# Performance work log

Measured on AMD Instinct MI355X. Metric: run time of the kernel, lower is better.

Reference implementation:

```python
import jax, jax.numpy as jnp
import numpy as np

B, S, HID, NH, HS = 4, 1024, 4096, 32, 128
ROT = 64  # rotary dim = head_size // 2 (ChatGLM partial rotary)
BLOCK_SIZE = 128


def setup_inputs() -> dict:
    key = jax.random.key(0)
    k0, k1, k2 = jax.random.split(key, 3)
    T = B * S
    hidden_states = jax.random.normal(k0, (T, HID), dtype=jnp.float32)
    w_qkv = jax.random.normal(k1, (HID, 3 * HID), dtype=jnp.float32) * 0.02
    b_qkv = jnp.zeros((3 * HID,), dtype=jnp.float32)
    w_dense = jax.random.normal(k2, (HID, HID), dtype=jnp.float32) * 0.02
    # real rotary tables: per-token position within its sequence
    inv_freq = 1.0 / (10000.0 ** (jnp.arange(0, ROT, 2, dtype=jnp.float32) / ROT))  # [ROT/2]
    pos = jnp.tile(jnp.arange(S, dtype=jnp.float32), B)  # [T]
    ang = pos[:, None] * inv_freq[None, :]  # [T, ROT/2]
    cos, sin = jnp.cos(ang), jnp.sin(ang)
    block_num = T // BLOCK_SIZE
    kv_cache_k = jnp.zeros((block_num, BLOCK_SIZE, NH, HS), dtype=jnp.float32)
    kv_cache_v = jnp.zeros((block_num, BLOCK_SIZE, NH, HS), dtype=jnp.float32)
    slots = jnp.arange(T, dtype=jnp.int32)
    return {"hidden_states": hidden_states, "cos": cos, "sin": sin,
            "w_qkv": w_qkv, "b_qkv": b_qkv, "w_dense": w_dense,
            "kv_cache_k": kv_cache_k, "kv_cache_v": kv_cache_v,
            "slots": slots, "batch": B, "seq_len": S}


def _rotary(x, cos, sin):
    # x: [T, NH, HS]; rotate-half over first ROT dims, pass-through the rest
    half = ROT // 2
    x1, x2, xp = x[..., :half], x[..., half:ROT], x[..., ROT:]
    c, s = cos[:, None, :], sin[:, None, :]
    return jnp.concatenate([x1 * c - x2 * s, x2 * c + x1 * s, xp], axis=-1)


def reference(hidden_states, cos, sin, w_qkv, b_qkv, w_dense,
              kv_cache_k, kv_cache_v, slots, batch, seq_len):
    T = hidden_states.shape[0]
    qkv = hidden_states @ w_qkv + b_qkv  # [T, 3*HID]
    q, k, v = jnp.split(qkv, 3, axis=1)
    q = q.reshape(T, NH, HS)
    k = k.reshape(T, NH, HS)
    v = v.reshape(T, NH, HS)
    q = _rotary(q, cos, sin)
    k = _rotary(k, cos, sin)
    # paged KV-cache scatter write (vectorized reshape_and_cache)
    bs = kv_cache_k.shape[1]
    bi, bo = slots // bs, slots % bs
    kv_k = kv_cache_k.at[bi, bo].set(k)
    kv_v = kv_cache_v.at[bi, bo].set(v)
    # prefill causal attention per sequence
    scale = HS ** -0.5
    q4 = q.reshape(batch, seq_len, NH, HS)
    k4 = k.reshape(batch, seq_len, NH, HS)
    v4 = v.reshape(batch, seq_len, NH, HS)
    scores = jnp.einsum("bqhd,bkhd->bhqk", q4, k4) * scale
    causal = jnp.tril(jnp.ones((seq_len, seq_len), dtype=bool))
    scores = jnp.where(causal[None, None], scores, jnp.finfo(scores.dtype).min)
    probs = jax.nn.softmax(scores, axis=-1)
    attn = jnp.einsum("bhqk,bkhd->bqhd", probs, v4).reshape(T, NH * HS)
    out = attn @ w_dense
    return out, kv_k, kv_v
```

## Files before the change

kernel.cpp:

```cpp
#include <hip/hip_runtime.h>

#define S_LEN 1024
#define NHEAD 32
#define HSZ   128
#define HIDN  4096
#define NQKV  12288
#define T_TOK 4096
#define ATT_SCALE 0.12751743f

typedef __bf16 bf16x8 __attribute__((ext_vector_type(8)));
typedef float  floatx4 __attribute__((ext_vector_type(4)));

union B8U { uint4 u; bf16x8 v; };

__device__ __forceinline__ unsigned short f2bf(float x) {
  unsigned int u = __float_as_uint(x);
  unsigned int r = (u + 0x7FFFu + ((u >> 16) & 1u)) >> 16;
  return (unsigned short)r;
}

__device__ __forceinline__ void gload_lds16(const void* g, void* l) {
  __builtin_amdgcn_global_load_lds(
      (__attribute__((address_space(1))) void*)(unsigned long long)g,
      (__attribute__((address_space(3))) void*)l, 16, 0, 0);
}

__device__ __forceinline__ bf16x8 lds_frag(const unsigned short* p) {
  return *reinterpret_cast<const bf16x8*>(p);
}

__global__ __launch_bounds__(256) void cast_bf16_kernel(
    const float* __restrict__ in, unsigned short* __restrict__ out, int n) {
  int idx = (blockIdx.x * 256 + threadIdx.x) * 4;
  if (idx >= n) return;
  float4 f = *reinterpret_cast<const float4*>(in + idx);
  ushort4 o;
  o.x = f2bf(f.x); o.y = f2bf(f.y); o.z = f2bf(f.z); o.w = f2bf(f.w);
  *reinterpret_cast<ushort4*>(out + idx) = o;
}

__global__ __launch_bounds__(256) void tcast_kernel(
    const float* __restrict__ w, unsigned short* __restrict__ wt, int K, int N) {
  __shared__ float tile[32][33];
  int n0 = blockIdx.x * 32, k0 = blockIdx.y * 32;
  int tx = threadIdx.x, ty = threadIdx.y;
#pragma unroll
  for (int i = 0; i < 32; i += 8)
    tile[ty + i][tx] = w[(size_t)(k0 + ty + i) * N + n0 + tx];
  __syncthreads();
#pragma unroll
  for (int i = 0; i < 32; i += 8)
    wt[(size_t)(n0 + ty + i) * K + k0 + tx] = f2bf(tile[tx][ty + i]);
}

__global__ __launch_bounds__(256) void gemm_bt(
    const unsigned short* __restrict__ A, const unsigned short* __restrict__ Bt,
    const float* __restrict__ bias, float* __restrict__ C, int M, int N, int K) {
  __shared__ __align__(16) unsigned short ldsA[128 * 32];
  __shared__ __align__(16) unsigned short ldsB[128 * 32];
  const int tid = threadIdx.x;
  const int lane = tid & 63, w = tid >> 6;
  const int m = lane & 15, quad = lane >> 4;
  const int wm = w >> 1, wn = w & 1;
  const int tM = blockIdx.y * 128, tN = blockIdx.x * 128;

  floatx4 acc[4][4] = {};
  const unsigned short* pA = A + (size_t)tM * K;
  const unsigned short* pB = Bt + (size_t)tN * K;
  const int r0 = tid >> 2, c0 = (tid & 3) * 8;

  for (int k0 = 0; k0 < K; k0 += 32) {
    gload_lds16(pA + (size_t)r0 * K + k0 + c0,        &ldsA[tid * 8]);
    gload_lds16(pA + (size_t)(r0 + 64) * K + k0 + c0, &ldsA[(tid + 256) * 8]);
    gload_lds16(pB + (size_t)r0 * K + k0 + c0,        &ldsB[tid * 8]);
    gload_lds16(pB + (size_t)(r0 + 64) * K + k0 + c0, &ldsB[(tid + 256) * 8]);
    __syncthreads();
    bf16x8 af[4], bfr[4];
#pragma unroll
    for (int i = 0; i < 4; ++i)
      af[i] = lds_frag(&ldsA[(wm * 64 + i * 16 + m) * 32 + quad * 8]);
#pragma unroll
    for (int j = 0; j < 4; ++j)
      bfr[j] = lds_frag(&ldsB[(wn * 64 + j * 16 + m) * 32 + quad * 8]);
#pragma unroll
    for (int i = 0; i < 4; ++i)
#pragma unroll
      for (int j = 0; j < 4; ++j)
        acc[i][j] = __builtin_amdgcn_mfma_f32_16x16x32_bf16(af[i], bfr[j], acc[i][j], 0, 0, 0);
    __syncthreads();
  }
#pragma unroll
  for (int i = 0; i < 4; ++i) {
    int row = tM + wm * 64 + i * 16 + quad * 4;
#pragma unroll
    for (int j = 0; j < 4; ++j) {
      int col = tN + wn * 64 + j * 16 + m;
      float bb = bias ? bias[col] : 0.0f;
      float* cp = C + (size_t)row * N + col;
#pragma unroll
      for (int r = 0; r < 4; ++r)
        cp[(size_t)r * N] = acc[i][j][r] + bb;
    }
  }
}

__global__ __launch_bounds__(256) void rope_kernel(
    const float* __restrict__ qkv, const float* __restrict__ cosb,
    const float* __restrict__ sinb, const int* __restrict__ slots,
    unsigned short* __restrict__ Qb, unsigned short* __restrict__ Kb,
    float* __restrict__ KvK, float* __restrict__ KvV) {
  const int t = blockIdx.x, tid = threadIdx.x;
  const size_t base = (size_t)t * NQKV;
  const int slot = slots[t];
  const size_t obase = (size_t)t * 4096;
  const size_t cbase = (size_t)slot * 4096;
  for (int idx = tid; idx < NHEAD * 32; idx += 256) {
    int hh = idx >> 5, r = idx & 31;
    float c = cosb[t * 32 + r], sn = sinb[t * 32 + r];
    int d0 = hh * 128 + r;
    float q1 = qkv[base + d0], q2 = qkv[base + d0 + 32];
    float k1 = qkv[base + 4096 + d0], k2 = qkv[base + 4096 + d0 + 32];
    float qr1 = q1 * c - q2 * sn, qr2 = q2 * c + q1 * sn;
    float kr1 = k1 * c - k2 * sn, kr2 = k2 * c + k1 * sn;
    Qb[obase + d0]      = f2bf(qr1 * ATT_SCALE);
    Qb[obase + d0 + 32] = f2bf(qr2 * ATT_SCALE);
    Kb[obase + d0]      = f2bf(kr1);
    Kb[obase + d0 + 32] = f2bf(kr2);
    KvK[cbase + d0] = kr1; KvK[cbase + d0 + 32] = kr2;
  }
  for (int idx = tid; idx < NHEAD * 64; idx += 256) {
    int hh = idx >> 6, p = idx & 63;
    int d = hh * 128 + 64 + p;
    float q = qkv[base + d], k = qkv[base + 4096 + d];
    Qb[obase + d] = f2bf(q * ATT_SCALE);
    Kb[obase + d] = f2bf(k);
    KvK[cbase + d] = k;
  }
  for (int idx = tid; idx < NHEAD * 128; idx += 256)
    KvV[cbase + idx] = qkv[base + 8192 + idx];
}

__global__ __launch_bounds__(256) void vtrans_kernel(
    const float* __restrict__ qkv, unsigned short* __restrict__ vt) {
  __shared__ float tile[32][33];
  int s0 = blockIdx.x * 32, d0 = blockIdx.y * 32, bh = blockIdx.z;
  int b = bh >> 5, h = bh & 31;
  int tx = threadIdx.x, ty = threadIdx.y;
#pragma unroll
  for (int i = 0; i < 32; i += 8)
    tile[ty + i][tx] =
        qkv[(size_t)(b * S_LEN + s0 + ty + i) * NQKV + 8192 + h * 128 + d0 + tx];
  __syncthreads();
#pragma unroll
  for (int i = 0; i < 32; i += 8)
    vt[(size_t)(bh * 128 + d0 + ty + i) * S_LEN + s0 + tx] = f2bf(tile[tx][ty + i]);
}

__global__ __launch_bounds__(256) void attn_kernel(
    const unsigned short* __restrict__ Q, const unsigned short* __restrict__ Kb,
    const unsigned short* __restrict__ Vt, unsigned short* __restrict__ Ob) {
  __shared__ __align__(16) unsigned short Ks[32][136];
  __shared__ __align__(16) unsigned short Vs[128][40];
  __shared__ __align__(16) unsigned short Pb[4][16][40];

  const int tid = threadIdx.x;
  const int w = tid >> 6, lane = tid & 63;
  const int m = lane & 15, quad = lane >> 4;
  const int qb = blockIdx.x, bh = blockIdx.y;
  const int b = bh >> 5, h = bh & 31;

  const int rowA = qb * 64 + w * 16 + m;
  const size_t qoff = ((size_t)(b * S_LEN + rowA)) * 4096 + h * 128;

  bf16x8 qf[4];
#pragma unroll
  for (int kc = 0; kc < 4; ++kc) {
    B8U t; t.u = *reinterpret_cast<const uint4*>(Q + qoff + kc * 32 + quad * 8);
    qf[kc] = t.v;
  }

  floatx4 O[8] = {};
  float m_run[4], l_run[4], alpha[4];
#pragma unroll
  for (int r = 0; r < 4; ++r) { m_run[r] = -3e38f; l_run[r] = 0.0f; }

  const int kend = qb * 64 + 63;
  for (int k0 = 0; k0 <= kend; k0 += 32) {
#pragma unroll
    for (int it = 0; it < 2; ++it) {
      int c = tid + it * 256;
      int key = c >> 4, d0 = (c & 15) * 8;
      uint4 val = *reinterpret_cast<const uint4*>(
          Kb + ((size_t)(b * S_LEN + k0 + key)) * 4096 + h * 128 + d0);
      *reinterpret_cast<uint4*>(&Ks[key][d0]) = val;
    }
#pragma unroll
    for (int it = 0; it < 2; ++it) {
      int c = tid + it * 256;
      int d = c >> 2, kk = (c & 3) * 8;
      uint4 val = *reinterpret_cast<const uint4*>(
          Vt + ((size_t)bh * 128 + d) * S_LEN + k0 + kk);
      *reinterpret_cast<uint4*>(&Vs[d][kk]) = val;
    }
    __syncthreads();

    floatx4 s[2];
#pragma unroll
    for (int t16 = 0; t16 < 2; ++t16) {
      floatx4 a = {};
#pragma unroll
      for (int kc = 0; kc < 4; ++kc) {
        bf16x8 kf = lds_frag(&Ks[t16 * 16 + m][kc * 32 + quad * 8]);
        a = __builtin_amdgcn_mfma_f32_16x16x32_bf16(qf[kc], kf, a, 0, 0, 0);
      }
      s[t16] = a;
    }

#pragma unroll
    for (int r = 0; r < 4; ++r) {
      int rowD = qb * 64 + w * 16 + quad * 4 + r;
      float s0 = s[0][r]; if (k0 + m > rowD)      s0 = -3e38f;
      float s1 = s[1][r]; if (k0 + 16 + m > rowD) s1 = -3e38f;
      float mx = fmaxf(s0, s1);
#pragma unroll
      for (int off = 8; off > 0; off >>= 1) mx = fmaxf(mx, __shfl_xor(mx, off));
      float mn = fmaxf(m_run[r], mx);
      float al = exp2f(m_run[r] - mn);
      float p0 = exp2f(s0 - mn), p1 = exp2f(s1 - mn);
      float rs = p0 + p1;
#pragma unroll
      for (int off = 8; off > 0; off >>= 1) rs += __shfl_xor(rs, off);
      l_run[r] = l_run[r] * al + rs;
      m_run[r] = mn; alpha[r] = al;
      Pb[w][quad * 4 + r][m]      = f2bf(p0);
      Pb[w][quad * 4 + r][16 + m] = f2bf(p1);
    }

#pragma unroll
    for (int nd = 0; nd < 8; ++nd)
#pragma unroll
      for (int r = 0; r < 4; ++r) O[nd][r] *= alpha[r];

    bf16x8 pf = lds_frag(&Pb[w][m][quad * 8]);
#pragma unroll
    for (int nd = 0; nd < 8; ++nd) {
      bf16x8 vf = lds_frag(&Vs[nd * 16 + m][quad * 8]);
      O[nd] = __builtin_amdgcn_mfma_f32_16x16x32_bf16(pf, vf, O[nd], 0, 0, 0);
    }
    __syncthreads();
  }

#pragma unroll
  for (int r = 0; r < 4; ++r) {
    int rowD = qb * 64 + w * 16 + quad * 4 + r;
    float inv = 1.0f / l_run[r];
    size_t obase = ((size_t)(b * S_LEN + rowD)) * 4096 + h * 128;
#pragma unroll
    for (int nd = 0; nd < 8; ++nd)
      Ob[obase + nd * 16 + m] = f2bf(O[nd][r] * inv);
  }
}

extern "C" void kernel_launch(void* const* d_in, const int* in_sizes, int n_in,
                              void* d_out, int out_size, void* d_ws, size_t ws_size,
                              hipStream_t stream) {
  const float* hidden  = (const float*)d_in[0];
  const float* cosb    = (const float*)d_in[1];
  const float* sinb    = (const float*)d_in[2];
  const float* w_qkv   = (const float*)d_in[3];
  const float* b_qkv   = (const float*)d_in[4];
  const float* w_dense = (const float*)d_in[5];
  const int*   slots   = (const int*)d_in[8];

  float* out = (float*)d_out;
  float* kvk = out + 16777216;
  float* kvv = out + 33554432;

  char* ws = (char*)d_ws;
  unsigned short* bfA = (unsigned short*)ws;
  unsigned short* Wt  = (unsigned short*)(ws + 33554432);
  float*          qkv = (float*)(ws + 134217728);
  unsigned short* Qb  = (unsigned short*)(ws + 335544320);
  unsigned short* Kb  = (unsigned short*)(ws + 369098752);
  unsigned short* Vt  = (unsigned short*)(ws + 402653184);

  cast_bf16_kernel<<<16384, 256, 0, stream>>>(hidden, bfA, T_TOK * HIDN);
  tcast_kernel<<<dim3(NQKV / 32, HIDN / 32), dim3(32, 8), 0, stream>>>(w_qkv, Wt, HIDN, NQKV);
  gemm_bt<<<dim3(NQKV / 128, T_TOK / 128), 256, 0, stream>>>(bfA, Wt, b_qkv, qkv, T_TOK, NQKV, HIDN);
  rope_kernel<<<T_TOK, 256, 0, stream>>>(qkv, cosb, sinb, slots, Qb, Kb, kvk, kvv);
  vtrans_kernel<<<dim3(S_LEN / 32, HSZ / 32, 128), dim3(32, 8), 0, stream>>>(qkv, Vt);
  attn_kernel<<<dim3(S_LEN / 64, 128), 256, 0, stream>>>(Qb, Kb, Vt, bfA);
  tcast_kernel<<<dim3(HIDN / 32, HIDN / 32), dim3(32, 8), 0, stream>>>(w_dense, Wt, HIDN, HIDN);
  gemm_bt<<<dim3(HIDN / 128, T_TOK / 128), 256, 0, stream>>>(bfA, Wt, nullptr, out, T_TOK, HIDN, HIDN);
}
```

Baseline: 1.561 ms.

## Replace 128x128 GEMM with pipelined 256x256 double-buffered swizzled LDS kernel

Replaces the simple 128x128-tile bf16 GEMM, which synchronised on every k-step, with a 256x256-tile, 512-thread kernel. It double-buffers LDS, issues staged async global-to-LDS loads interleaved with MFMA quarters, uses XOR-swizzled LDS layout to avoid bank conflicts, remaps workgroups for XCD/L2 locality, and raises wave priority during MFMA bursts. The goal is to hide memory latency and improve data reuse in both projection GEMMs. The cost is more LDS (128KB per block) and register pressure, plus fragile hand-placed waitcnt and barrier logic.

Measured after the change: 1.317 ms. 15.6% less time.

```diff
diff --git a/kernel.cpp b/kernel.cpp
--- a/kernel.cpp
+++ b/kernel.cpp
@@ -53,55 +53,162 @@
     wt[(size_t)(n0 + ty + i) * K + k0 + tx] = f2bf(tile[tx][ty + i]);
 }
 
-__global__ __launch_bounds__(256) void gemm_bt(
+__global__ __launch_bounds__(512, 2) void gemm256(
     const unsigned short* __restrict__ A, const unsigned short* __restrict__ Bt,
-    const float* __restrict__ bias, float* __restrict__ C, int M, int N, int K) {
-  __shared__ __align__(16) unsigned short ldsA[128 * 32];
-  __shared__ __align__(16) unsigned short ldsB[128 * 32];
+    const float* __restrict__ bias, float* __restrict__ C,
+    int N, int K, int NBX) {
+  __shared__ __align__(16) unsigned short ldsA[2][16384];
+  __shared__ __align__(16) unsigned short ldsB[2][16384];
+
   const int tid = threadIdx.x;
   const int lane = tid & 63, w = tid >> 6;
   const int m = lane & 15, quad = lane >> 4;
-  const int wm = w >> 1, wn = w & 1;
-  const int tM = blockIdx.y * 128, tN = blockIdx.x * 128;
-
-  floatx4 acc[4][4] = {};
+  const int wm = w >> 2, wn = w & 3;
+
+  const int nwg = gridDim.x;
+  const int orig = blockIdx.x;
+  const int id = (orig & 7) * (nwg >> 3) + (orig >> 3);
+  const int by = id / NBX, bx = id - by * NBX;
+  const int tM = by << 8, tN = bx << 8;
+  const int NT = K >> 6;
+
   const unsigned short* pA = A + (size_t)tM * K;
   const unsigned short* pB = Bt + (size_t)tN * K;
-  const int r0 = tid >> 2, c0 = (tid & 3) * 8;
-
-  for (int k0 = 0; k0 < K; k0 += 32) {
-    gload_lds16(pA + (size_t)r0 * K + k0 + c0,        &ldsA[tid * 8]);
-    gload_lds16(pA + (size_t)(r0 + 64) * K + k0 + c0, &ldsA[(tid + 256) * 8]);
-    gload_lds16(pB + (size_t)r0 * K + k0 + c0,        &ldsB[tid * 8]);
-    gload_lds16(pB + (size_t)(r0 + 64) * K + k0 + c0, &ldsB[(tid + 256) * 8]);
-    __syncthreads();
-    bf16x8 af[4], bfr[4];
-#pragma unroll
-    for (int i = 0; i < 4; ++i)
-      af[i] = lds_frag(&ldsA[(wm * 64 + i * 16 + m) * 32 + quad * 8]);
-#pragma unroll
-    for (int j = 0; j < 4; ++j)
-      bfr[j] = lds_frag(&ldsB[(wn * 64 + j * 16 + m) * 32 + quad * 8]);
-#pragma unroll
-    for (int i = 0; i < 4; ++i)
-#pragma unroll
-      for (int j = 0; j < 4; ++j)
-        acc[i][j] = __builtin_amdgcn_mfma_f32_16x16x32_bf16(af[i], bfr[j], acc[i][j], 0, 0, 0);
-    __syncthreads();
-  }
-#pragma unroll
-  for (int i = 0; i < 4; ++i) {
-    int row = tM + wm * 64 + i * 16 + quad * 4;
-#pragma unroll
-    for (int j = 0; j < 4; ++j) {
-      int col = tN + wn * 64 + j * 16 + m;
-      float bb = bias ? bias[col] : 0.0f;
-      float* cp = C + (size_t)row * N + col;
-#pragma unroll
-      for (int r = 0; r < 4; ++r)
-        cp[(size_t)r * N] = acc[i][j][r] + bb;
-    }
-  }
+
+  size_t goff0;
+  {
+    int o = tid * 16;
+    int blk = o >> 10;
+    int r = (o >> 6) & 15;
+    int cB = (o & 63) ^ (((r >> 3) & 1) << 5);
+    goff0 = (size_t)((blk >> 1) * 16 + r) * K + ((blk & 1) << 5) + (cB >> 1);
+  }
+  const size_t goff1 = goff0 + (size_t)64 * K;
+  const int ldst0 = tid * 16;
+
+  const int innerOff = (m << 6) + (((quad * 8) ^ (((m >> 3) & 1) << 4)) << 1);
+
+  floatx4 acc[2][2][4][2] = {};
+
+  auto STAGE = [&](int s) {
+    if (s < 4 * NT) {
+      const int tt = s >> 2, slot = s & 3;
+      const int buf = tt & 1;
+      const int half = (slot == 1 || slot == 2) ? 1 : 0;
+      const unsigned short* g =
+          ((slot & 1) ? pB : pA) + (size_t)(half << 7) * K + (tt << 6);
+      char* l = (char*)((slot & 1) ? ldsB[buf] : ldsA[buf]) + (half << 14);
+      gload_lds16(g + goff0, l + ldst0);
+      gload_lds16(g + goff1, l + ldst0 + 8192);
+    }
+  };
+
+  auto FRAG = [&](const unsigned short* tile, int br, int kk) -> bf16x8 {
+    return *reinterpret_cast<const bf16x8*>(
+        (const char*)tile + ((((br << 1) + kk) << 10) + innerOff));
+  };
+
+  auto MQ = [&](floatx4 (&ac)[4][2], bf16x8 (&aa)[4][2], bf16x8 (&bb)[2][2]) {
+#pragma unroll
+    for (int kk = 0; kk < 2; ++kk)
+#pragma unroll
+      for (int i = 0; i < 4; ++i)
+#pragma unroll
+        for (int j = 0; j < 2; ++j)
+          ac[i][j] = __builtin_amdgcn_mfma_f32_16x16x32_bf16(
+              aa[i][kk], bb[j][kk], ac[i][j], 0, 0, 0);
+  };
+
+#pragma unroll
+  for (int s = 0; s < 7; ++s) STAGE(s);
+  asm volatile("s_waitcnt vmcnt(6)" ::: "memory");
+  __builtin_amdgcn_s_barrier();
+  asm volatile("" ::: "memory");
+
+#pragma unroll 2
+  for (int t = 0; t < NT; ++t) {
+    const unsigned short* lA = ldsA[t & 1];
+    const unsigned short* lB = ldsB[t & 1];
+    const int P = t << 2;
+    bf16x8 a[4][2], b0[2][2], b1[2][2];
+
+#pragma unroll
+    for (int i = 0; i < 4; ++i) {
+      a[i][0] = FRAG(lA, wm * 4 + i, 0);
+      a[i][1] = FRAG(lA, wm * 4 + i, 1);
+    }
+#pragma unroll
+    for (int j = 0; j < 2; ++j) {
+      b0[j][0] = FRAG(lB, wn * 2 + j, 0);
+      b0[j][1] = FRAG(lB, wn * 2 + j, 1);
+    }
+    STAGE(P + 7);
+    __builtin_amdgcn_s_barrier();
+    asm volatile("s_waitcnt lgkmcnt(0)" ::: "memory");
+    __builtin_amdgcn_s_setprio(1);
+    MQ(acc[0][0], a, b0);
+    __builtin_amdgcn_s_setprio(0);
+    __builtin_amdgcn_s_barrier();
+
+#pragma unroll
+    for (int j = 0; j < 2; ++j) {
+      b1[j][0] = FRAG(lB, wn * 2 + 8 + j, 0);
+      b1[j][1] = FRAG(lB, wn * 2 + 8 + j, 1);
+    }
+    STAGE(P + 8);
+    __builtin_amdgcn_s_barrier();
+    asm volatile("s_waitcnt lgkmcnt(0)" ::: "memory");
+    __builtin_amdgcn_s_setprio(1);
+    MQ(acc[0][1], a, b1);
+    __builtin_amdgcn_s_setprio(0);
+    __builtin_amdgcn_s_barrier();
+
+#pragma unroll
+    for (int i = 0; i < 4; ++i) {
+      a[i][0] = FRAG(lA, wm * 4 + 8 + i, 0);
+      a[i][1] = FRAG(lA, wm * 4 + 8 + i, 1);
+    }
+    STAGE(P + 9);
+    __builtin_amdgcn_s_barrier();
+    asm volatile("s_waitcnt lgkmcnt(0)" ::: "memory");
+    __builtin_amdgcn_s_setprio(1);
+    MQ(acc[1][1], a, b1);
+    __builtin_amdgcn_s_setprio(0);
+    __builtin_amdgcn_s_barrier();
+
+#pragma unroll
+    for (int j = 0; j < 2; ++j) {
+      b0[j][0] = FRAG(lB, wn * 2 + j, 0);
+      b0[j][1] = FRAG(lB, wn * 2 + j, 1);
+    }
+    STAGE(P + 10);
+    __builtin_amdgcn_s_barrier();
+    asm volatile("s_waitcnt lgkmcnt(0)" ::: "memory");
+    __builtin_amdgcn_s_setprio(1);
+    MQ(acc[1][0], a, b0);
+    __builtin_amdgcn_s_setprio(0);
+    if (t + 2 < NT) asm volatile("s_waitcnt vmcnt(6)" ::: "memory");
+    else            asm volatile("s_waitcnt vmcnt(0)" ::: "memory");
+    __builtin_amdgcn_s_barrier();
+    asm volatile("" ::: "memory");
+  }
+
+#pragma unroll
+  for (int rh = 0; rh < 2; ++rh)
+#pragma unroll
+    for (int ch = 0; ch < 2; ++ch)
+#pragma unroll
+      for (int i = 0; i < 4; ++i)
+#pragma unroll
+        for (int j = 0; j < 2; ++j) {
+          const int row = tM + wm * 64 + rh * 128 + i * 16 + quad * 4;
+          const int col = tN + wn * 32 + ch * 128 + j * 16 + m;
+          const float bb = bias ? bias[col] : 0.0f;
+          float* cp = C + (size_t)row * N + col;
+#pragma unroll
+          for (int rr = 0; rr < 4; ++rr)
+            cp[(size_t)rr * N] = acc[rh][ch][i][j][rr] + bb;
+        }
 }
 
 __global__ __launch_bounds__(256) void rope_kernel(
@@ -286,10 +393,12 @@
 
   cast_bf16_kernel<<<16384, 256, 0, stream>>>(hidden, bfA, T_TOK * HIDN);
   tcast_kernel<<<dim3(NQKV / 32, HIDN / 32), dim3(32, 8), 0, stream>>>(w_qkv, Wt, HIDN, NQKV);
-  gemm_bt<<<dim3(NQKV / 128, T_TOK / 128), 256, 0, stream>>>(bfA, Wt, b_qkv, qkv, T_TOK, NQKV, HIDN);
+  gemm256<<<dim3((T_TOK / 256) * (NQKV / 256)), 512, 0, stream>>>(
+      bfA, Wt, b_qkv, qkv, NQKV, HIDN, NQKV / 256);
   rope_kernel<<<T_TOK, 256, 0, stream>>>(qkv, cosb, sinb, slots, Qb, Kb, kvk, kvv);
   vtrans_kernel<<<dim3(S_LEN / 32, HSZ / 32, 128), dim3(32, 8), 0, stream>>>(qkv, Vt);
   attn_kernel<<<dim3(S_LEN / 64, 128), 256, 0, stream>>>(Qb, Kb, Vt, bfA);
   tcast_kernel<<<dim3(HIDN / 32, HIDN / 32), dim3(32, 8), 0, stream>>>(w_dense, Wt, HIDN, HIDN);
-  gemm_bt<<<dim3(HIDN / 128, T_TOK / 128), 256, 0, stream>>>(bfA, Wt, nullptr, out, T_TOK, HIDN, HIDN);
-}
+  gemm256<<<dim3((T_TOK / 256) * (HIDN / 256)), 512, 0, stream>>>(
+      bfA, Wt, nullptr, out, HIDN, HIDN, HIDN / 256);
+}
```
